# Kernel optimization log

Hardware: AMD Instinct MI355X
Metric: run time of the kernel (lower is better)

The kernel has to match this reference:

```python
import jax, jax.numpy as jnp
import numpy as np

B, T, E, D, A, O, L = 16, 512, 1024, 1024, 1024, 10000, 128
SOS = EOS = O - 1
SCALING = 2.0  # AttDot softmax scaling in espnet of this era


def setup_inputs() -> dict:
    key = jax.random.key(0)
    ks = jax.random.split(key, 16)
    s = 0.05
    inp = {
        "hpad": jax.random.normal(ks[0], (B, T, E), jnp.float32),
        "hlen": jnp.full((B,), T, dtype=jnp.int32),
        "ys": jax.random.randint(ks[1], (B, L), 0, O - 2).astype(jnp.int32),
        "embed_w": jax.random.normal(ks[2], (O, D), jnp.float32) * s,
        "att_Wenc": jax.random.normal(ks[3], (E, A), jnp.float32) * s,
        "att_Wdec": jax.random.normal(ks[4], (D, A), jnp.float32) * s,
        "W_ih0": jax.random.normal(ks[5], (4 * D, D + E), jnp.float32) * s,
        "W_hh0": jax.random.normal(ks[6], (4 * D, D), jnp.float32) * s,
        "b_ih0": jnp.zeros((4 * D,), jnp.float32),
        "b_hh0": jnp.zeros((4 * D,), jnp.float32),
        "W_ih1": jax.random.normal(ks[7], (4 * D, D), jnp.float32) * s,
        "W_hh1": jax.random.normal(ks[8], (4 * D, D), jnp.float32) * s,
        "b_ih1": jnp.zeros((4 * D,), jnp.float32),
        "b_hh1": jnp.zeros((4 * D,), jnp.float32),
        "W_out": jax.random.normal(ks[9], (D, O), jnp.float32) * s,
        "b_out": jnp.zeros((O,), jnp.float32),
    }
    return inp


def _lstm_cell(x, h, c, W_ih, W_hh, b_ih, b_hh):
    g = x @ W_ih.T + b_ih + h @ W_hh.T + b_hh
    i, f, gg, o = jnp.split(g, 4, axis=-1)
    c_new = jax.nn.sigmoid(f) * c + jax.nn.sigmoid(i) * jnp.tanh(gg)
    h_new = jax.nn.sigmoid(o) * jnp.tanh(c_new)
    return h_new, c_new


def reference(hpad, hlen, ys, embed_w, att_Wenc, att_Wdec,
              W_ih0, W_hh0, b_ih0, b_hh0, W_ih1, W_hh1, b_ih1, b_hh1,
              W_out, b_out):
    b, t, e = hpad.shape
    d = W_hh0.shape[1]
    # mask_by_length(hpad, hlen, 0)
    mask = (jnp.arange(t)[None, :] < hlen[:, None])
    hpad_m = hpad * mask[..., None].astype(hpad.dtype)

    # sos/eos padding: pad_ys_in = [sos; y], pad_ys_out = [y; eos]
    sos_col = jnp.full((b, 1), SOS, dtype=ys.dtype)
    eos_col = jnp.full((b, 1), EOS, dtype=ys.dtype)
    ys_in = jnp.concatenate([sos_col, ys], axis=1)   # [B, L+1]
    ys_out = jnp.concatenate([ys, eos_col], axis=1)  # [B, L+1]
    olength = ys_in.shape[1]

    eys = embed_w[ys_in]                 # [B, L+1, D]
    pre_enc = jnp.tanh(jnp.einsum('bte,ea->bta', hpad_m, att_Wenc))  # [B,T,A]

    def step(carry, ey):
        z0, c0, z1, c1 = carry
        # AttDot: e = sum(tanh(Wenc h) * tanh(Wdec z0)); w = softmax(2*e)
        dq = jnp.tanh(z0 @ att_Wdec)                        # [B, A]
        escore = jnp.einsum('bta,ba->bt', pre_enc, dq)      # [B, T]
        w = jax.nn.softmax(SCALING * escore, axis=1)
        att_c = jnp.einsum('bt,bte->be', w, hpad_m)         # [B, E]
        x0 = jnp.concatenate([ey, att_c], axis=1)           # [B, D+E]
        z0, c0 = _lstm_cell(x0, z0, c0, W_ih0, W_hh0, b_ih0, b_hh0)
        z1, c1 = _lstm_cell(z0, z1, c1, W_ih1, W_hh1, b_ih1, b_hh1)
        return (z0, c0, z1, c1), z1

    zeros = jnp.zeros((b, d), hpad.dtype)
    carry0 = (zeros, zeros, zeros, zeros)
    _, z_all = jax.lax.scan(step, carry0, jnp.swapaxes(eys, 0, 1))  # [L+1, B, D]
    z_all = jnp.swapaxes(z_all, 0, 1).reshape(b * olength, d)

    logits = z_all @ W_out + b_out                          # [B*(L+1), O]
    labels = ys_out.reshape(-1)
    logp = jax.nn.log_softmax(logits, axis=-1)
    nll = -jnp.take_along_axis(logp, labels[:, None], axis=1)[:, 0]
    # all sequences have length L, no ignore_id padding; loss *= mean(len(ys_in)) - 1 = L
    loss = jnp.mean(nll) * jnp.float32(olength - 1)
    acc = jnp.mean((jnp.argmax(logits, axis=-1) == labels).astype(jnp.float32))
    return loss, acc
```

## Files before the change

### kernel.cpp

```cpp
#include <hip/hip_runtime.h>
#include <math.h>

#define NB 16
#define NT 512
#define NE 1024
#define ND 1024
#define NA 1024
#define NO 10000
#define NL 128
#define NOL 129
#define NROWS (NB*NOL)
#define TOK_SOS 9999
#define TOK_EOS 9999
#define NBLK 256

typedef unsigned short u16;
typedef unsigned int u32;
typedef __bf16 bf16x8 __attribute__((ext_vector_type(8)));
typedef float f32x4 __attribute__((ext_vector_type(4)));
typedef unsigned short u16x8 __attribute__((ext_vector_type(8)));
typedef unsigned short u16x4 __attribute__((ext_vector_type(4)));

__device__ __forceinline__ float sigf(float x){ return 1.0f/(1.0f+expf(-x)); }
__device__ __forceinline__ float b2f(u16 s){
  union { u32 i; float f; } u; u.i = ((u32)s) << 16; return u.f;
}
__device__ __forceinline__ u16 f2b(float f){
  union { float f; u32 i; } u; u.f = f;
  u32 r = u.i + 0x7FFFu + ((u.i >> 16) & 1u);
  return (u16)(r >> 16);
}
__device__ __forceinline__ float dot8(bf16x8 a, bf16x8 b){
  float s = 0.f;
  #pragma unroll
  for (int j=0;j<8;++j) s += (float)a[j]*(float)b[j];
  return s;
}

__device__ __forceinline__ void coh_stf(float* p, float v){
  __hip_atomic_store(p, v, __ATOMIC_RELAXED, __HIP_MEMORY_SCOPE_AGENT);
}
__device__ __forceinline__ u32 coh_ldu(const u32* p){
  return __hip_atomic_load((u32*)p, __ATOMIC_RELAXED, __HIP_MEMORY_SCOPE_AGENT);
}
__device__ __forceinline__ void coh_stu(u32* p, u32 v){
  __hip_atomic_store(p, v, __ATOMIC_RELAXED, __HIP_MEMORY_SCOPE_AGENT);
}

__global__ void zero4_kernel(uint4* __restrict__ p, int n){
  int i = blockIdx.x*256 + threadIdx.x;
  if (i < n) p[i] = make_uint4(0,0,0,0);
}

__global__ __launch_bounds__(256) void cvt5_kernel(
    const float* __restrict__ Wih0, const float* __restrict__ Whh0,
    const float* __restrict__ Wih1, const float* __restrict__ Whh1,
    u16* __restrict__ w0c, u16* __restrict__ wh0,
    u16* __restrict__ w1c, u16* __restrict__ wh1, u16* __restrict__ w0e){
  const float* src; int ld, off; u16* dst;
  switch (blockIdx.y){
    case 0:  src = Wih0; ld = 2048; off = 1024; dst = w0c; break;
    case 1:  src = Whh0; ld = 1024; off = 0;    dst = wh0; break;
    case 2:  src = Wih1; ld = 1024; off = 0;    dst = w1c; break;
    case 3:  src = Whh1; ld = 1024; off = 0;    dst = wh1; break;
    default: src = Wih0; ld = 2048; off = 0;    dst = w0e; break;
  }
  int i = (blockIdx.x*256 + threadIdx.x)*4;
  int row = i >> 10, col = i & 1023;
  float4 v = *(const float4*)(src + (size_t)row*ld + off + col);
  u16x4 o = { f2b(v.x), f2b(v.y), f2b(v.z), f2b(v.w) };
  *(u16x4*)(dst + i) = o;
}

__global__ __launch_bounds__(256) void tcvt_kernel(
    const float* __restrict__ src, int R, int C, u16* __restrict__ dst){
  __shared__ float tile[32][33];
  const int c0 = blockIdx.x*32, r0 = blockIdx.y*32;
  const int tx = threadIdx.x & 31, ty = threadIdx.x >> 5;
  #pragma unroll
  for (int k = 0; k < 4; ++k){
    int rr = ty + k*8;
    int c = c0 + tx;
    float v = (c < C) ? src[(size_t)(r0+rr)*C + c] : 0.0f;
    tile[rr][tx] = v;
  }
  __syncthreads();
  #pragma unroll
  for (int k = 0; k < 4; ++k){
    int cc = ty + k*8;
    dst[(size_t)(c0+cc)*R + r0 + tx] = f2b(tile[tx][cc]);
  }
}

__global__ __launch_bounds__(256) void hpadbf_kernel(
    const float* __restrict__ hpad, const int* __restrict__ hlen, u16* __restrict__ dst){
  int i = (blockIdx.x*256 + threadIdx.x)*4;
  int bt = i >> 10;
  int b = bt >> 9, tt = bt & 511;
  float4 v = *(const float4*)(hpad + (size_t)i);
  float m = (tt < hlen[b]) ? 1.0f : 0.0f;
  u16x4 o = { f2b(v.x*m), f2b(v.y*m), f2b(v.z*m), f2b(v.w*m) };
  *(u16x4*)(dst + i) = o;
}

__global__ __launch_bounds__(256) void hpadT_kernel(
    const float* __restrict__ hpad, const int* __restrict__ hlen, u16* __restrict__ dst){
  __shared__ float tile[32][33];
  const int e0 = blockIdx.x*32, t0 = blockIdx.y*32, b = blockIdx.z;
  const int tx = threadIdx.x & 31, ty = threadIdx.x >> 5;
  const int len = hlen[b];
  #pragma unroll
  for (int k = 0; k < 4; ++k){
    int r = ty + k*8;
    tile[r][tx] = hpad[((size_t)b*512 + t0 + r)*1024 + e0 + tx];
  }
  __syncthreads();
  #pragma unroll
  for (int k = 0; k < 4; ++k){
    int el = ty + k*8;
    float m = (t0 + tx < len) ? 1.0f : 0.0f;
    dst[((size_t)b*1024 + e0 + el)*512 + t0 + tx] = f2b(tile[tx][el]*m);
  }
}

__global__ void bias_add_kernel(const float* __restrict__ a, const float* __restrict__ b,
                                float* __restrict__ o){
  int i = blockIdx.x*256 + threadIdx.x;
  if (i < 4096) o[i] = a[i] + b[i];
}

__global__ __launch_bounds__(256) void eys_kernel(
    const int* __restrict__ ys, const float* __restrict__ embed, u16* __restrict__ eys){
  int row = blockIdx.x;
  int c = threadIdx.x*4;
  if (row < NROWS){
    int b = row / NOL, l = row - b*NOL;
    int tok = (l==0) ? TOK_SOS : ys[b*NL + l - 1];
    float4 v = *(const float4*)(embed + (size_t)tok*1024 + c);
    u16x4 o = { f2b(v.x), f2b(v.y), f2b(v.z), f2b(v.w) };
    *(u16x4*)(eys + (size_t)row*1024 + c) = o;
  } else {
    u16x4 o = {0,0,0,0};
    *(u16x4*)(eys + (size_t)row*1024 + c) = o;
  }
}

#define GEMM128_BODY(Aptr, Bptr) \
  const int tid = threadIdx.x, lane = tid & 63, wv = tid >> 6; \
  const int r = lane & 15, q = lane >> 4; \
  const int m0 = blockIdx.x*128, n0 = blockIdx.y*128; \
  const int ar0 = m0 + wv*32 + r; \
  f32x4 acc[2][8]; \
  _Pragma("unroll") \
  for (int a = 0; a < 2; ++a) \
    _Pragma("unroll") \
    for (int s = 0; s < 8; ++s) acc[a][s] = (f32x4){0.f,0.f,0.f,0.f}; \
  const u16* a0p = (Aptr) + (size_t)ar0*1024 + q*8; \
  const u16* a1p = a0p + 16*1024; \
  const u16* bp  = (Bptr) + (size_t)(n0 + r)*1024 + q*8; \
  for (int kt = 0; kt < 32; ++kt){ \
    bf16x8 av0 = *(const bf16x8*)(a0p + kt*32); \
    bf16x8 av1 = *(const bf16x8*)(a1p + kt*32); \
    _Pragma("unroll") \
    for (int s = 0; s < 8; ++s){ \
      bf16x8 bv = *(const bf16x8*)(bp + (size_t)s*16384 + kt*32); \
      acc[0][s] = __builtin_amdgcn_mfma_f32_16x16x32_bf16(av0, bv, acc[0][s], 0,0,0); \
      acc[1][s] = __builtin_amdgcn_mfma_f32_16x16x32_bf16(av1, bv, acc[1][s], 0,0,0); \
    } \
  }

__global__ __launch_bounds__(256) void preenc_g(
    const u16* __restrict__ hpadbf, const u16* __restrict__ wencT, u16* __restrict__ pre){
  GEMM128_BODY(hpadbf, wencT)
  #pragma unroll
  for (int a = 0; a < 2; ++a)
    #pragma unroll
    for (int s = 0; s < 8; ++s)
      #pragma unroll
      for (int rr = 0; rr < 4; ++rr){
        int row = m0 + wv*32 + a*16 + q*4 + rr, col = n0 + s*16 + r;
        pre[(size_t)row*1024 + col] = f2b(tanhf(acc[a][s][rr]));
      }
}

__global__ __launch_bounds__(256) void gey_g(
    const u16* __restrict__ eys, const u16* __restrict__ w0e,
    const float* __restrict__ bih0, const float* __restrict__ bhh0, u16* __restrict__ gey){
  GEMM128_BODY(eys, w0e)
  #pragma unroll
  for (int a = 0; a < 2; ++a)
    #pragma unroll
    for (int s = 0; s < 8; ++s)
      #pragma unroll
      for (int rr = 0; rr < 4; ++rr){
        int row = m0 + wv*32 + a*16 + q*4 + rr, col = n0 + s*16 + r;
        if (row < NROWS)
          gey[(size_t)row*4096 + col] = f2b(acc[a][s][rr] + bih0[col] + bhh0[col]);
      }
}

__global__ __launch_bounds__(256) void logits_g(
    const u16* __restrict__ zallb, const u16* __restrict__ woutT,
    const float* __restrict__ bout, u16* __restrict__ logits){
  GEMM128_BODY(zallb, woutT)
  #pragma unroll
  for (int a = 0; a < 2; ++a)
    #pragma unroll
    for (int s = 0; s < 8; ++s)
      #pragma unroll
      for (int rr = 0; rr < 4; ++rr){
        int row = m0 + wv*32 + a*16 + q*4 + rr, col = n0 + s*16 + r;
        if (row < NROWS && col < NO)
          logits[(size_t)row*NO + col] = f2b(acc[a][s][rr] + bout[col]);
      }
}

__device__ __forceinline__ void gbar(u32* af, int epoch){
  __syncthreads();
  if (blockIdx.x == 0){
    int w = threadIdx.x;
    if (w > 0){
      while (coh_ldu(&af[w << 5]) < (u32)epoch) __builtin_amdgcn_s_sleep(1);
    }
    __syncthreads();
    if (threadIdx.x == 0) coh_stu(&af[0], (u32)epoch);
  } else {
    if (threadIdx.x == 0){
      coh_stu(&af[blockIdx.x << 5], (u32)epoch);
      while (coh_ldu(&af[0]) < (u32)epoch) __builtin_amdgcn_s_sleep(1);
    }
    __syncthreads();
  }
}

__device__ __forceinline__ void group_bar(u32* gfl, int epoch){
  __syncthreads();
  if (threadIdx.x == 0) coh_stu(&gfl[blockIdx.x << 5], (u32)epoch);
  const int base = blockIdx.x & ~15;
  if ((int)threadIdx.x < 16){
    while ((int)coh_ldu(&gfl[(base + threadIdx.x) << 5]) < epoch) __builtin_amdgcn_s_sleep(1);
  }
  __syncthreads();
}

__device__ __forceinline__ f32x4 tile_gemm(const u16* lw, const u16* ab){
  f32x4 acc = {0.f,0.f,0.f,0.f};
  #pragma unroll
  for (int kt = 0; kt < 16; ++kt){
    bf16x8 a = *(const bf16x8*)(ab + kt*32);
    bf16x8 b = *(const bf16x8*)(lw + kt*512);
    acc = __builtin_amdgcn_mfma_f32_16x16x32_bf16(a, b, acc, 0, 0, 0);
  }
  return acc;
}

__global__ __launch_bounds__(256, 1) void seq_kernel(
    const u16* __restrict__ pre,
    const u16* __restrict__ hpadT,
    const u16* __restrict__ w0c, const u16* __restrict__ wh0,
    const u16* __restrict__ w1c, const u16* __restrict__ wh1,
    const u16* __restrict__ wdecT,
    const u16* __restrict__ gey,
    const float* __restrict__ bias1,
    const int* __restrict__ hlen,
    u16* dqr,
    float* escr,
    u16* attcr,
    u16* z0r,
    u16* z1r,
    u16* zallb,
    u32* af, u32* gfl)
{
  __builtin_amdgcn_fence(__ATOMIC_ACQUIRE, "agent");

  const int wg = blockIdx.x, tid = threadIdx.x;
  const int lane = tid & 63, wv = tid >> 6;
  const int r = lane & 15, q = lane >> 4;

  extern __shared__ __align__(16) u16 dynlds[];
  u16* lw1 = dynlds;
  u16* lw0 = dynlds + 32768;
  __shared__ float sred8[8];
  __shared__ float sw[512];
  __shared__ float spart[4][64];
  __shared__ float gex[4][16][16];
  __shared__ float sdq[16*16*4];

  const int dg16 = (wg & 63)*16, sub4 = (wg >> 6)*4;

  #pragma unroll
  for (int it = 0; it < 16; ++it){
    int m = tid + it*256;
    int kb = m >> 4, c = m & 15;
    int k0 = kb*8;
    int gi = c >> 2;
    int d  = dg16 + sub4 + (c & 3);
    size_t gr = (size_t)(gi*1024 + d)*1024;
    const u16* s1 = (k0 < 1024) ? (w1c + gr + k0) : (wh1 + gr + k0 - 1024);
    const u16* s0 = (k0 < 1024) ? (w0c + gr + k0) : (wh0 + gr + k0 - 1024);
    *(u16x8*)(lw1 + (m << 3)) = *(const u16x8*)s1;
    *(u16x8*)(lw0 + (m << 3)) = *(const u16x8*)s0;
  }
  __syncthreads();

  float c0r = 0.f, c1r = 0.f;
  int epoch = 1;
  const int lwoff = ((wv*64 + q)*16 + r) << 3;

  for (int t = 0; t <= NOL; ++t){
    const u16* z0t = z0r + (size_t)t*16384;
    u16* dq_t   = dqr   + (size_t)t*16384;
    float* esc_t= escr  + (size_t)t*8192;
    u16* attc_t = attcr + (size_t)t*16384;

    if (t >= 1){
      const int s = t - 1;
      const u16* z1p = z1r + (size_t)(t-1)*16384;
      const u16* ab = ((wv < 2) ? z0t : z1p) + r*1024 + (wv & 1)*512 + q*8;
      f32x4 acc = tile_gemm(lw1 + lwoff, ab);
      #pragma unroll
      for (int rr = 0; rr < 4; ++rr) gex[wv][q*4+rr][r] = acc[rr];
      __syncthreads();
      if (tid < 64){
        int b = tid >> 2, dd = tid & 3, d = dg16 + sub4 + dd;
        float g0 = gex[0][b][0*4+dd] + gex[1][b][0*4+dd] + gex[2][b][0*4+dd] + gex[3][b][0*4+dd];
        float g1 = gex[0][b][1*4+dd] + gex[1][b][1*4+dd] + gex[2][b][1*4+dd] + gex[3][b][1*4+dd];
        float g2 = gex[0][b][2*4+dd] + gex[1][b][2*4+dd] + gex[2][b][2*4+dd] + gex[3][b][2*4+dd];
        float g3 = gex[0][b][3*4+dd] + gex[1][b][3*4+dd] + gex[2][b][3*4+dd] + gex[3][b][3*4+dd];
        g0 += bias1[d]; g1 += bias1[1024+d]; g2 += bias1[2048+d]; g3 += bias1[3072+d];
        float cn = sigf(g1)*c1r + sigf(g0)*tanhf(g2);
        float zn = sigf(g3)*tanhf(cn);
        c1r = cn;
        float zn2 = __shfl_down(zn, 1);
        if ((tid & 1) == 0){
          u32 pk = (u32)f2b(zn) | ((u32)f2b(zn2) << 16);
          *(u32*)(zallb + ((size_t)b*NOL + s)*1024 + d) = pk;
          coh_stu((u32*)(z1r + (size_t)t*16384 + b*1024 + d), pk);
        }
      }
      __syncthreads();
    }
    if (t < NOL){
      const int b = tid & 15, ks = tid >> 4;
      float a4[4] = {0.f,0.f,0.f,0.f};
      #pragma unroll
      for (int i = 0; i < 8; ++i){
        bf16x8 za = *(const bf16x8*)(z0t + b*1024 + ks*64 + i*8);
        #pragma unroll
        for (int nn = 0; nn < 4; ++nn){
          bf16x8 wb = *(const bf16x8*)(wdecT + (size_t)(wg*4+nn)*1024 + ks*64 + i*8);
          a4[nn] += dot8(za, wb);
        }
      }
      #pragma unroll
      for (int nn = 0; nn < 4; ++nn) sdq[(ks*16 + b)*4 + nn] = a4[nn];
      __syncthreads();
      if (tid < 64){
        int b2 = tid >> 2, nn = tid & 3;
        float s2 = 0.f;
        #pragma unroll
        for (int ks2 = 0; ks2 < 16; ++ks2) s2 += sdq[(ks2*16 + b2)*4 + nn];
        float dv = tanhf(s2);
        float dv2 = __shfl_down(dv, 1);
        if ((tid & 1) == 0){
          u32 pk = (u32)f2b(dv) | ((u32)f2b(dv2) << 16);
          coh_stu((u32*)(dq_t + b2*1024 + wg*4 + nn), pk);
        }
      }
    }
    gbar(af, epoch++);
    if (t == NOL) break;

    {
      const int rbase = wg*32 + wv*8;
      const int b = (wg*32) >> 9;
      const u16* dqb = dq_t + b*1024 + lane*16;
      u16x8 d0 = *(const u16x8*)(dqb);
      u16x8 d1 = *(const u16x8*)(dqb + 8);
      float qv[16];
      #pragma unroll
      for (int j = 0; j < 8; ++j){ qv[j] = b2f(d0[j]); qv[8+j] = b2f(d1[j]); }
      #pragma unroll
      for (int rr = 0; rr < 8; ++rr){
        const u16* pr = pre + (size_t)(rbase+rr)*1024 + lane*16;
        u16x8 p0 = *(const u16x8*)(pr);
        u16x8 p1 = *(const u16x8*)(pr+8);
        float acc = 0.f;
        #pragma unroll
        for (int j = 0; j < 8; ++j){
          acc += b2f(p0[j])*qv[j];
          acc += b2f(p1[j])*qv[8+j];
        }
        #pragma unroll
        for (int off = 32; off > 0; off >>= 1) acc += __shfl_xor(acc, off, 64);
        if (lane == 0) coh_stf(&esc_t[rbase+rr], 2.0f*acc);
      }
    }
    group_bar(gfl, epoch++);

    {
      const int b = wg >> 4, ec = wg & 15;
      const int len = hlen[b];
      float e0 = (tid < len)     ? esc_t[b*512 + tid]       : -INFINITY;
      float e1 = (tid+256 < len) ? esc_t[b*512 + tid + 256] : -INFINITY;
      float mloc = fmaxf(e0, e1);
      #pragma unroll
      for (int off = 32; off > 0; off >>= 1) mloc = fmaxf(mloc, __shfl_xor(mloc, off, 64));
      if (lane == 0) sred8[wv] = mloc;
      __syncthreads();
      float mx = fmaxf(fmaxf(sred8[0], sred8[1]), fmaxf(sred8[2], sred8[3]));
      float p0 = (tid < len)     ? expf(e0 - mx) : 0.0f;
      float p1 = (tid+256 < len) ? expf(e1 - mx) : 0.0f;
      float sloc = p0 + p1;
      #pragma unroll
      for (int off = 32; off > 0; off >>= 1) sloc += __shfl_xor(sloc, off, 64);
      if (lane == 0) sred8[4 + wv] = sloc;
      __syncthreads();
      float inv = 1.0f/(sred8[4] + sred8[5] + sred8[6] + sred8[7]);
      sw[tid] = p0*inv; sw[tid+256] = p1*inv;
      __syncthreads();
      const int el = tid & 63, th = tid >> 6;
      const u16* hp = hpadT + ((size_t)b*1024 + ec*64 + el)*512 + th*128;
      float acc = 0.f;
      #pragma unroll
      for (int i = 0; i < 16; ++i){
        u16x8 v = *(const u16x8*)(hp + i*8);
        #pragma unroll
        for (int j = 0; j < 8; ++j) acc += sw[th*128 + i*8 + j]*b2f(v[j]);
      }
      spart[th][el] = acc;
      __syncthreads();
      if (tid < 64){
        float s2 = spart[0][tid]+spart[1][tid]+spart[2][tid]+spart[3][tid];
        float s2n = __shfl_down(s2, 1);
        if ((tid & 1) == 0){
          u32 pk = (u32)f2b(s2) | ((u32)f2b(s2n) << 16);
          coh_stu((u32*)(attc_t + b*1024 + ec*64 + tid), pk);
        }
      }
    }
    gbar(af, epoch++);

    {
      const u16* ab = ((wv < 2) ? attc_t : z0t) + r*1024 + (wv & 1)*512 + q*8;
      f32x4 acc = tile_gemm(lw0 + lwoff, ab);
      #pragma unroll
      for (int rr = 0; rr < 4; ++rr) gex[wv][q*4+rr][r] = acc[rr];
      __syncthreads();
      if (tid < 64){
        int b = tid >> 2, dd = tid & 3, d = dg16 + sub4 + dd;
        const u16* gr = gey + ((size_t)b*NOL + t)*4096 + d;
        float g0 = gex[0][b][0*4+dd] + gex[1][b][0*4+dd] + gex[2][b][0*4+dd] + gex[3][b][0*4+dd];
        float g1 = gex[0][b][1*4+dd] + gex[1][b][1*4+dd] + gex[2][b][1*4+dd] + gex[3][b][1*4+dd];
        float g2 = gex[0][b][2*4+dd] + gex[1][b][2*4+dd] + gex[2][b][2*4+dd] + gex[3][b][2*4+dd];
        float g3 = gex[0][b][3*4+dd] + gex[1][b][3*4+dd] + gex[2][b][3*4+dd] + gex[3][b][3*4+dd];
        g0 += b2f(gr[0]); g1 += b2f(gr[1024]); g2 += b2f(gr[2048]); g3 += b2f(gr[3072]);
        float cn = sigf(g1)*c0r + sigf(g0)*tanhf(g2);
        float zn = sigf(g3)*tanhf(cn);
        c0r = cn;
        float zn2 = __shfl_down(zn, 1);
        if ((tid & 1) == 0){
          u32 pk = (u32)f2b(zn) | ((u32)f2b(zn2) << 16);
          coh_stu((u32*)(z0r + (size_t)(t+1)*16384 + b*1024 + d), pk);
        }
      }
    }
    gbar(af, epoch++);
  }
}

__global__ __launch_bounds__(256) void loss_kernel(
    const u16* __restrict__ logits, const int* __restrict__ ys, float* __restrict__ accum){
  int row = blockIdx.x;
  int tid = threadIdx.x;
  const u16* lr = logits + (size_t)row * NO;
  __shared__ float sm[256], ss[256];
  __shared__ int   si[256];
  float m = -INFINITY, s = 0.f; int mi = 0x7FFFFFFF;
  for (int n = tid; n < NO; n += 256){
    float v = b2f(lr[n]);
    if (v > m){
      s = s*__expf(m - v) + 1.0f;
      m = v; mi = n;
    } else {
      s += __expf(v - m);
    }
  }
  sm[tid] = m; ss[tid] = s; si[tid] = mi;
  __syncthreads();
  for (int st = 128; st > 0; st >>= 1){
    if (tid < st){
      float m1 = sm[tid], s1 = ss[tid]; int i1 = si[tid];
      float m2 = sm[tid+st], s2 = ss[tid+st]; int i2 = si[tid+st];
      float M = fmaxf(m1, m2);
      ss[tid] = s1*__expf(m1 - M) + s2*__expf(m2 - M);
      sm[tid] = M;
      si[tid] = (m1 > m2) ? i1 : (m2 > m1) ? i2 : min(i1, i2);
    }
    __syncthreads();
  }
  if (tid == 0){
    int b = row / NOL, l = row - b*NOL;
    int label = (l < NL) ? ys[b*NL + l] : TOK_EOS;
    float lse = sm[0] + logf(ss[0]);
    float nll = lse - b2f(lr[label]);
    atomicAdd(&accum[0], nll);
    atomicAdd(&accum[1], (si[0]==label) ? 1.0f : 0.0f);
  }
}

__global__ void finalize_kernel(const float* __restrict__ accum, float* __restrict__ out){
  out[0] = accum[0] / (float)NROWS * (float)(NOL-1);
  out[1] = accum[1] / (float)NROWS;
}

extern "C" void kernel_launch(void* const* d_in, const int* in_sizes, int n_in,
                              void* d_out, int out_size, void* d_ws, size_t ws_size,
                              hipStream_t stream){
  const float* hpad  = (const float*)d_in[0];
  const int*   hlen  = (const int*)  d_in[1];
  const int*   ys    = (const int*)  d_in[2];
  const float* embed = (const float*)d_in[3];
  const float* Wenc  = (const float*)d_in[4];
  const float* Wdec  = (const float*)d_in[5];
  const float* Wih0  = (const float*)d_in[6];
  const float* Whh0  = (const float*)d_in[7];
  const float* bih0  = (const float*)d_in[8];
  const float* bhh0  = (const float*)d_in[9];
  const float* Wih1  = (const float*)d_in[10];
  const float* Whh1  = (const float*)d_in[11];
  const float* bih1  = (const float*)d_in[12];
  const float* bhh1  = (const float*)d_in[13];
  const float* Wout  = (const float*)d_in[14];
  const float* bout  = (const float*)d_in[15];
  float* out = (float*)d_out;

  char* ws = (char*)d_ws;
  size_t cur = 0;
  auto alloc = [&](size_t bytes) -> char* {
    char* p = ws + cur;
    cur += (bytes + 255) & ~(size_t)255;
    return p;
  };
  u16*   pre_bf   = (u16*)  alloc(16777216);
  u16*   hpadT    = (u16*)  alloc(16777216);
  u16*   w0c      = (u16*)  alloc(8388608);
  u16*   wh0      = (u16*)  alloc(8388608);
  u16*   w1c      = (u16*)  alloc(8388608);
  u16*   wh1      = (u16*)  alloc(8388608);
  u16*   wdecT    = (u16*)  alloc(2097152);
  u16*   wencT    = (u16*)  alloc(2097152);
  u16*   woutT    = (u16*)  alloc(20709376);
  u16*   gey      = (u16*)  alloc(16908288);
  u16*   zallb    = (u16*)  alloc(4456448);
  u16*   logits   = (u16*)  alloc(41280000);
  float* bias1    = (float*)alloc(16384);
  u16*   dqr      = (u16*)  alloc(129u*32768);
  float* escr     = (float*)alloc(129u*32768);
  u16*   attcr    = (u16*)  alloc(129u*32768);
  u16*   z0r      = (u16*)  alloc(130u*32768);
  u16*   z1r      = (u16*)  alloc(130u*32768);
  u32*   af       = (u32*)  alloc(32768);
  u32*   gfl      = (u32*)  alloc(32768);
  float* accum    = (float*)alloc(128);

  u16*   hpad_bf  = (u16*)logits;
  u16*   eys      = (u16*)(logits + 8388608);
  u16*   w0e      = (u16*)(logits + 11165696);

  zero4_kernel<<<17, 256, 0, stream>>>((uint4*)af, 4104);
  zero4_kernel<<<8, 256, 0, stream>>>((uint4*)z0r, 2048);
  zero4_kernel<<<8, 256, 0, stream>>>((uint4*)z1r, 2048);

  tcvt_kernel<<<dim3(32,32),  256, 0, stream>>>(Wenc, 1024, 1024, wencT);
  tcvt_kernel<<<dim3(32,32),  256, 0, stream>>>(Wdec, 1024, 1024, wdecT);
  tcvt_kernel<<<dim3(316,32), 256, 0, stream>>>(Wout, 1024, NO,   woutT);
  cvt5_kernel<<<dim3(4096,5), 256, 0, stream>>>(Wih0, Whh0, Wih1, Whh1,
                                                w0c, wh0, w1c, wh1, w0e);
  hpadbf_kernel<<<8192, 256, 0, stream>>>(hpad, hlen, hpad_bf);
  hpadT_kernel<<<dim3(32,16,16), 256, 0, stream>>>(hpad, hlen, hpadT);
  bias_add_kernel<<<16, 256, 0, stream>>>(bih1, bhh1, bias1);
  eys_kernel<<<2176, 256, 0, stream>>>(ys, embed, eys);

  preenc_g<<<dim3(64, 8),  256, 0, stream>>>(hpad_bf, wencT, pre_bf);
  gey_g   <<<dim3(17, 32), 256, 0, stream>>>(eys, w0e, bih0, bhh0, gey);

  hipFuncSetAttribute((const void*)seq_kernel,
                      hipFuncAttributeMaxDynamicSharedMemorySize, 131072);
  seq_kernel<<<NBLK, 256, 131072, stream>>>(pre_bf, hpadT, w0c, wh0, w1c, wh1,
                                            wdecT, gey, bias1, hlen,
                                            dqr, escr, attcr, z0r, z1r, zallb, af, gfl);

  logits_g<<<dim3(17, 79), 256, 0, stream>>>(zallb, woutT, bout, logits);
  loss_kernel<<<NROWS, 256, 0, stream>>>(logits, ys, accum);
  finalize_kernel<<<1, 1, 0, stream>>>(accum, out);
}
```

Baseline: 3.513 ms.

## Split grid barrier into arrive/fin phases and overlap recurrent GEMM halves

Splits the software grid barrier into arrive, mid and finish phases. Waves whose GEMM inputs are already available (z0 recurrent half for layer 0, previous z1 for layer 1) compute their tile while the barrier is still pending, which hides part of the LSTM matmul behind the cross-block synchronisation latency. Epochs are now computed from t instead of a running counter. The change relies on those inputs being final before the barrier completes, and it makes the barrier protocol more intricate.

After: 5.832 ms. +66.0%, slower.

```diff
diff --git a/kernel.cpp b/kernel.cpp
--- a/kernel.cpp
+++ b/kernel.cpp
@@ -215,22 +215,30 @@
       }
 }
 
-__device__ __forceinline__ void gbar(u32* af, int epoch){
-  __syncthreads();
+__device__ __forceinline__ void bar_arrive(u32* af, int e){
+  __syncthreads();
+  if (blockIdx.x != 0 && threadIdx.x == 0) coh_stu(&af[blockIdx.x << 5], (u32)e);
+}
+__device__ __forceinline__ void bar_mid(u32* af, int e){
   if (blockIdx.x == 0){
     int w = threadIdx.x;
     if (w > 0){
-      while (coh_ldu(&af[w << 5]) < (u32)epoch) __builtin_amdgcn_s_sleep(1);
+      while ((int)coh_ldu(&af[w << 5]) < e) __builtin_amdgcn_s_sleep(1);
     }
     __syncthreads();
-    if (threadIdx.x == 0) coh_stu(&af[0], (u32)epoch);
-  } else {
+    if (threadIdx.x == 0) coh_stu(&af[0], (u32)e);
+  }
+}
+__device__ __forceinline__ void bar_fin(u32* af, int e){
+  if (blockIdx.x != 0){
     if (threadIdx.x == 0){
-      coh_stu(&af[blockIdx.x << 5], (u32)epoch);
-      while (coh_ldu(&af[0]) < (u32)epoch) __builtin_amdgcn_s_sleep(1);
-    }
-    __syncthreads();
-  }
+      while ((int)coh_ldu(&af[0]) < e) __builtin_amdgcn_s_sleep(1);
+    }
+  }
+  __syncthreads();
+}
+__device__ __forceinline__ void gbar(u32* af, int e){
+  bar_arrive(af, e); bar_mid(af, e); bar_fin(af, e);
 }
 
 __device__ __forceinline__ void group_bar(u32* gfl, int epoch){
@@ -304,7 +312,6 @@
   __syncthreads();
 
   float c0r = 0.f, c1r = 0.f;
-  int epoch = 1;
   const int lwoff = ((wv*64 + q)*16 + r) << 3;
 
   for (int t = 0; t <= NOL; ++t){
@@ -313,13 +320,21 @@
     float* esc_t= escr  + (size_t)t*8192;
     u16* attc_t = attcr + (size_t)t*16384;
 
+    f32x4 accA = {0.f,0.f,0.f,0.f};
+    if (t >= 1 && wv >= 2){
+      const u16* z1p = z1r + (size_t)(t-1)*16384;
+      const u16* ab = z1p + r*1024 + (wv & 1)*512 + q*8;
+      accA = tile_gemm(lw1 + lwoff, ab);
+    }
+    if (t > 0) bar_fin(af, 3*t);
     if (t >= 1){
       const int s = t - 1;
-      const u16* z1p = z1r + (size_t)(t-1)*16384;
-      const u16* ab = ((wv < 2) ? z0t : z1p) + r*1024 + (wv & 1)*512 + q*8;
-      f32x4 acc = tile_gemm(lw1 + lwoff, ab);
-      #pragma unroll
-      for (int rr = 0; rr < 4; ++rr) gex[wv][q*4+rr][r] = acc[rr];
+      if (wv < 2){
+        const u16* ab = z0t + r*1024 + (wv & 1)*512 + q*8;
+        accA = tile_gemm(lw1 + lwoff, ab);
+      }
+      #pragma unroll
+      for (int rr = 0; rr < 4; ++rr) gex[wv][q*4+rr][r] = accA[rr];
       __syncthreads();
       if (tid < 64){
         int b = tid >> 2, dd = tid & 3, d = dg16 + sub4 + dd;
@@ -340,7 +355,8 @@
       }
       __syncthreads();
     }
-    if (t < NOL){
+    if (t == NOL) break;
+    {
       const int b = tid & 15, ks = tid >> 4;
       float a4[4] = {0.f,0.f,0.f,0.f};
       #pragma unroll
@@ -368,8 +384,7 @@
         }
       }
     }
-    gbar(af, epoch++);
-    if (t == NOL) break;
+    gbar(af, 3*t + 1);
 
     {
       const int rbase = wg*32 + wv*8;
@@ -396,7 +411,7 @@
         if (lane == 0) coh_stf(&esc_t[rbase+rr], 2.0f*acc);
       }
     }
-    group_bar(gfl, epoch++);
+    group_bar(gfl, t + 1);
 
     {
       const int b = wg >> 4, ec = wg & 15;
@@ -439,13 +454,22 @@
         }
       }
     }
-    gbar(af, epoch++);
+    bar_arrive(af, 3*t + 2);
+    bar_mid(af, 3*t + 2);
+    f32x4 accD = {0.f,0.f,0.f,0.f};
+    if (wv >= 2){
+      const u16* ab = z0t + r*1024 + (wv & 1)*512 + q*8;
+      accD = tile_gemm(lw0 + lwoff, ab);
+    }
+    bar_fin(af, 3*t + 2);
 
     {
-      const u16* ab = ((wv < 2) ? attc_t : z0t) + r*1024 + (wv & 1)*512 + q*8;
-      f32x4 acc = tile_gemm(lw0 + lwoff, ab);
-      #pragma unroll
-      for (int rr = 0; rr < 4; ++rr) gex[wv][q*4+rr][r] = acc[rr];
+      if (wv < 2){
+        const u16* ab = attc_t + r*1024 + (wv & 1)*512 + q*8;
+        accD = tile_gemm(lw0 + lwoff, ab);
+      }
+      #pragma unroll
+      for (int rr = 0; rr < 4; ++rr) gex[wv][q*4+rr][r] = accD[rr];
       __syncthreads();
       if (tid < 64){
         int b = tid >> 2, dd = tid & 3, d = dg16 + sub4 + dd;
@@ -465,7 +489,8 @@
         }
       }
     }
-    gbar(af, epoch++);
+    bar_arrive(af, 3*t + 3);
+    bar_mid(af, 3*t + 3);
   }
 }
 
```
